# Optimization experiments

Hardware: AMD Instinct MI355X
Metric: run time of the kernel (lower is better)

Reference implementation:

```python
import jax, jax.numpy as jnp
import numpy as np
import math

B, T, D = 2, 2048, 1024
NH = 16
HD = D // NH


def setup_inputs() -> dict:
    key = jax.random.key(0)
    k1, k2, k3 = jax.random.split(key, 3)
    scale = 0.02
    x = jax.random.normal(k1, (B, T, D), dtype=jnp.float32)
    Wqkv = jax.random.normal(k2, (D, 3 * D), dtype=jnp.float32) * scale
    bqkv = jnp.zeros((3 * D,), dtype=jnp.float32)
    Wproj = jax.random.normal(k3, (D, D), dtype=jnp.float32) * scale
    bproj = jnp.zeros((D,), dtype=jnp.float32)
    return {"x": x, "Wqkv": Wqkv, "bqkv": bqkv, "Wproj": Wproj, "bproj": bproj}


def reference(x, Wqkv, bqkv, Wproj, bproj):
    b, t, c = x.shape
    qkv = x @ Wqkv + bqkv                      # [B,T,3D]
    q, k, v = jnp.split(qkv, 3, axis=2)
    # [B,T,NH,HD] -> [B,NH,T,HD]
    q = q.reshape(b, t, NH, HD).transpose(0, 2, 1, 3)
    k = k.reshape(b, t, NH, HD).transpose(0, 2, 1, 3)
    v = v.reshape(b, t, NH, HD).transpose(0, 2, 1, 3)
    att = jnp.einsum('bhqd,bhkd->bhqk', q, k) / math.sqrt(HD)  # [B,NH,T,T]
    causal = jnp.tril(jnp.ones((t, t), dtype=bool))
    att = jnp.where(causal, att, -jnp.inf)
    att = jax.nn.softmax(att, axis=-1)
    y = jnp.einsum('bhqk,bhkd->bhqd', att, v)  # [B,NH,T,HD]
    y = y.transpose(0, 2, 1, 3).reshape(b, t, c)
    return y @ Wproj + bproj
```

## Files before the change

kernel.cpp:

```cpp
#include <hip/hip_runtime.h>
#include <hip/hip_bf16.h>

#define B_   2
#define T_   2048
#define D_   1024
#define NH_  16
#define HD_  64
#define MROWS (B_*T_)
#define HEADELEMS (B_*NH_*T_*HD_)

#define QSCALE 0.180336880f

typedef unsigned short u16;
typedef unsigned int   u32;

typedef float f32x4  __attribute__((ext_vector_type(4)));
typedef short bf16x8 __attribute__((ext_vector_type(8)));

__device__ __forceinline__ float bf2f(u16 v) {
    return __uint_as_float(((u32)v) << 16);
}
__device__ __forceinline__ u16 f2bf(float f) {
    u32 x = __float_as_uint(f);
    u32 r = (x + 0x7fffu + ((x >> 16) & 1u)) >> 16;
    return (u16)r;
}

__global__ __launch_bounds__(256)
void conv_kernel(const float* __restrict__ in, u16* __restrict__ out, int n4)
{
    int i = blockIdx.x * 256 + threadIdx.x;
    if (i >= n4) return;
    float4 v = ((const float4*)in)[i];
    ushort4 o;
    o.x = f2bf(v.x); o.y = f2bf(v.y); o.z = f2bf(v.z); o.w = f2bf(v.w);
    ((ushort4*)out)[i] = o;
}

__global__ __launch_bounds__(256)
void transpose_conv_kernel(const float* __restrict__ in, u16* __restrict__ out,
                           int K, int N)
{
    __shared__ float Ts[64][65];
    const int t  = threadIdx.x;
    const int n0 = blockIdx.x * 64;
    const int k0 = blockIdx.y * 64;

    #pragma unroll
    for (int pass = 0; pass < 4; pass++) {
        const int r = pass * 16 + (t >> 4);
        const int c = (t & 15) * 4;
        float4 v = *(const float4*)(in + (size_t)(k0 + r) * N + n0 + c);
        Ts[r][c] = v.x; Ts[r][c+1] = v.y; Ts[r][c+2] = v.z; Ts[r][c+3] = v.w;
    }
    __syncthreads();
    #pragma unroll
    for (int pass = 0; pass < 2; pass++) {
        const int nn = pass * 32 + (t >> 3);
        const int kk = (t & 7) * 8;
        u16 o[8];
        #pragma unroll
        for (int j = 0; j < 8; j++) o[j] = f2bf(Ts[kk + j][nn]);
        *(uint4*)(out + (size_t)(n0 + nn) * K + k0 + kk) = *(const uint4*)o;
    }
}

template <int MODE>
__global__ __launch_bounds__(256)
void gemm_mfma(const u16* __restrict__ A, const u16* __restrict__ BT,
               const float* __restrict__ bias, void* __restrict__ outv,
               int M, int N, int K)
{
    __shared__ u16 As[128][40];
    __shared__ u16 Bs[128][40];

    const int t    = threadIdx.x;
    const int wave = t >> 6;
    const int lane = t & 63;
    const int l16  = lane & 15;
    const int quad = lane >> 4;

    const int m0 = blockIdx.y * 128;
    const int n0 = blockIdx.x * 128;
    const int mb = (wave >> 1) * 64;
    const int nb = (wave & 1) * 64;

    const int srow = t >> 2;
    const int skk  = (t & 3) * 8;

    f32x4 acc[4][4];
    #pragma unroll
    for (int i = 0; i < 4; i++)
        #pragma unroll
        for (int j = 0; j < 4; j++) acc[i][j] = (f32x4){0,0,0,0};

    for (int k0 = 0; k0 < K; k0 += 32) {
        __syncthreads();
        #pragma unroll
        for (int pass = 0; pass < 2; pass++) {
            const int r = srow + pass * 64;
            uint4 va = *(const uint4*)(A  + (size_t)(m0 + r) * K + k0 + skk);
            *(uint4*)&As[r][skk] = va;
            uint4 vb = *(const uint4*)(BT + (size_t)(n0 + r) * K + k0 + skk);
            *(uint4*)&Bs[r][skk] = vb;
        }
        __syncthreads();

        bf16x8 af[4], bfr[4];
        #pragma unroll
        for (int i = 0; i < 4; i++)
            af[i] = *(const bf16x8*)&As[mb + i*16 + l16][quad * 8];
        #pragma unroll
        for (int j = 0; j < 4; j++)
            bfr[j] = *(const bf16x8*)&Bs[nb + j*16 + l16][quad * 8];

        #pragma unroll
        for (int i = 0; i < 4; i++)
            #pragma unroll
            for (int j = 0; j < 4; j++)
                acc[i][j] = __builtin_amdgcn_mfma_f32_16x16x32_bf16(
                    af[i], bfr[j], acc[i][j], 0, 0, 0);
    }

    #pragma unroll
    for (int j = 0; j < 4; j++) {
        const int n = n0 + nb + j*16 + l16;
        const float bv = bias[n];
        #pragma unroll
        for (int i = 0; i < 4; i++) {
            #pragma unroll
            for (int r = 0; r < 4; r++) {
                const int m = m0 + mb + i*16 + quad*4 + r;
                float v = acc[i][j][r] + bv;
                if (MODE == 0) {
                    ((float*)outv)[(size_t)m * N + n] = v;
                } else {
                    const int b   = m >> 11;
                    const int tt  = m & 2047;
                    const int sec = n >> 10;
                    const int dd  = n & 1023;
                    const int h   = dd >> 6;
                    const int hd  = dd & 63;
                    const size_t hbase = ((size_t)(b*NH_ + h)) * T_ * HD_;
                    size_t idx;
                    if (sec == 2)
                        idx = (size_t)2 * HEADELEMS + hbase + (size_t)hd * T_ + tt;
                    else
                        idx = (size_t)sec * HEADELEMS + hbase + (size_t)tt * HD_ + hd;
                    if (sec == 0) v *= QSCALE;
                    ((u16*)outv)[idx] = f2bf(v);
                }
            }
        }
    }
}

__global__ __launch_bounds__(256)
void attn_mfma_kernel(const u16* __restrict__ Q, const u16* __restrict__ K,
                      const u16* __restrict__ VT, u16* __restrict__ y1)
{
    __shared__ u16 Ks[2][64][72];
    __shared__ u16 Vs[2][64][72];
    __shared__ u16 Plds[4][32][72];

    const int t    = threadIdx.x;
    const int wave = t >> 6;
    const int lane = t & 63;
    const int l16  = lane & 15;
    const int quad = lane >> 4;

    const int hb = blockIdx.x;
    const int yy = blockIdx.y;
    const int qt = (yy < 8) ? (15 - yy) : (yy - 8);
    const int b  = hb >> 4;
    const int h  = hb & 15;
    const size_t base = (size_t)hb * T_ * HD_;

    const int qw0 = qt * 128 + wave * 32;

    bf16x8 qf[2][2];
    #pragma unroll
    for (int mi = 0; mi < 2; mi++) {
        const u16* qp = Q + base + (size_t)(qw0 + mi*16 + l16) * HD_ + quad * 8;
        qf[mi][0] = *(const bf16x8*)(qp);
        qf[mi][1] = *(const bf16x8*)(qp + 32);
    }

    bf16x8 onesf;
    #pragma unroll
    for (int i = 0; i < 8; i++) onesf[i] = (short)0x3F80;

    f32x4 o[2][4];
    #pragma unroll
    for (int mi = 0; mi < 2; mi++)
        #pragma unroll
        for (int d = 0; d < 4; d++) o[mi][d] = (f32x4){0,0,0,0};
    f32x4 accl[2] = {(f32x4){0,0,0,0}, (f32x4){0,0,0,0}};

    u16 (*P)[72] = Plds[wave];

    const int nsteps  = 2 * qt + 2;
    const int tiles_w = (qw0 + 32 + 63) >> 6;

    const int srow = t >> 3;
    const int scol = (t & 7) * 8;

    uint4 kr0, kr1, vr0, vr1;
    {
        const u16* kp = K + base + (size_t)srow * HD_ + scol;
        kr0 = *(const uint4*)kp;
        kr1 = *(const uint4*)(kp + 32 * HD_);
        const u16* vp = VT + base + (size_t)srow * T_ + scol;
        vr0 = *(const uint4*)vp;
        vr1 = *(const uint4*)(vp + 32 * T_);
        *(uint4*)&Ks[0][srow][scol]      = kr0;
        *(uint4*)&Ks[0][srow + 32][scol] = kr1;
        *(uint4*)&Vs[0][srow][scol]      = vr0;
        *(uint4*)&Vs[0][srow + 32][scol] = vr1;
    }
    __syncthreads();

    for (int kt = 0; kt < nsteps; kt++) {
        const int cur = kt & 1;
        const int k0  = kt * 64;
        const bool have_next = (kt + 1 < nsteps);

        if (have_next) {
            const u16* kp = K + base + (size_t)(k0 + 64 + srow) * HD_ + scol;
            kr0 = *(const uint4*)kp;
            kr1 = *(const uint4*)(kp + 32 * HD_);
            const u16* vp = VT + base + (size_t)srow * T_ + k0 + 64 + scol;
            vr0 = *(const uint4*)vp;
            vr1 = *(const uint4*)(vp + 32 * T_);
        }

        if (kt < tiles_w) {
            f32x4 s[2][4];
            #pragma unroll
            for (int j = 0; j < 4; j++) {
                bf16x8 kf0 = *(const bf16x8*)&Ks[cur][j*16 + l16][quad * 8];
                bf16x8 kf1 = *(const bf16x8*)&Ks[cur][j*16 + l16][32 + quad * 8];
                #pragma unroll
                for (int mi = 0; mi < 2; mi++) {
                    f32x4 z = {0,0,0,0};
                    z = __builtin_amdgcn_mfma_f32_16x16x32_bf16(qf[mi][0], kf0, z, 0, 0, 0);
                    s[mi][j] = __builtin_amdgcn_mfma_f32_16x16x32_bf16(qf[mi][1], kf1, z, 0, 0, 0);
                }
            }

            #pragma unroll
            for (int mi = 0; mi < 2; mi++) {
                const int rmin = qw0 + mi * 16;
                const bool need_mask = (k0 + 63 > rmin);
                #pragma unroll
                for (int r = 0; r < 4; r++) {
                    const int qi = rmin + quad * 4 + r;
                    #pragma unroll
                    for (int j = 0; j < 4; j++) {
                        float e = __builtin_amdgcn_exp2f(s[mi][j][r]);
                        if (need_mask && (k0 + j*16 + l16 > qi)) e = 0.f;
                        P[mi*16 + quad*4 + r][j*16 + l16] =
                            (u16)((__float_as_uint(e) + 0x8000u) >> 16);
                    }
                }
            }

            bf16x8 pf[2][2];
            #pragma unroll
            for (int mi = 0; mi < 2; mi++) {
                pf[mi][0] = *(const bf16x8*)&P[mi*16 + l16][quad * 8];
                pf[mi][1] = *(const bf16x8*)&P[mi*16 + l16][32 + quad * 8];
            }

            #pragma unroll
            for (int mi = 0; mi < 2; mi++) {
                accl[mi] = __builtin_amdgcn_mfma_f32_16x16x32_bf16(pf[mi][0], onesf, accl[mi], 0, 0, 0);
                accl[mi] = __builtin_amdgcn_mfma_f32_16x16x32_bf16(pf[mi][1], onesf, accl[mi], 0, 0, 0);
            }

            #pragma unroll
            for (int d = 0; d < 4; d++) {
                bf16x8 v0 = *(const bf16x8*)&Vs[cur][d*16 + l16][quad * 8];
                bf16x8 v1 = *(const bf16x8*)&Vs[cur][d*16 + l16][32 + quad * 8];
                #pragma unroll
                for (int mi = 0; mi < 2; mi++) {
                    o[mi][d] = __builtin_amdgcn_mfma_f32_16x16x32_bf16(pf[mi][0], v0, o[mi][d], 0, 0, 0);
                    o[mi][d] = __builtin_amdgcn_mfma_f32_16x16x32_bf16(pf[mi][1], v1, o[mi][d], 0, 0, 0);
                }
            }
        }

        if (have_next) {
            const int nxt = cur ^ 1;
            *(uint4*)&Ks[nxt][srow][scol]      = kr0;
            *(uint4*)&Ks[nxt][srow + 32][scol] = kr1;
            *(uint4*)&Vs[nxt][srow][scol]      = vr0;
            *(uint4*)&Vs[nxt][srow + 32][scol] = vr1;
            __syncthreads();
        }
    }

    #pragma unroll
    for (int mi = 0; mi < 2; mi++) {
        #pragma unroll
        for (int r = 0; r < 4; r++) {
            const float inv = 1.f / accl[mi][r];
            const int qi = qw0 + mi*16 + quad*4 + r;
            u16* yp = y1 + ((size_t)(b * T_ + qi)) * D_ + h * HD_ + l16;
            yp[0]  = f2bf(o[mi][0][r] * inv);
            yp[16] = f2bf(o[mi][1][r] * inv);
            yp[32] = f2bf(o[mi][2][r] * inv);
            yp[48] = f2bf(o[mi][3][r] * inv);
        }
    }
}

extern "C" void kernel_launch(void* const* d_in, const int* in_sizes, int n_in,
                              void* d_out, int out_size, void* d_ws, size_t ws_size,
                              hipStream_t stream)
{
    const float* x     = (const float*)d_in[0];
    const float* Wqkv  = (const float*)d_in[1];
    const float* bqkv  = (const float*)d_in[2];
    const float* Wproj = (const float*)d_in[3];
    const float* bproj = (const float*)d_in[4];

    u16* scratch = (u16*)d_out;
    u16* xb      = scratch;
    u16* WqkvT   = scratch + (size_t)MROWS * D_;

    u16* qkv = (u16*)d_ws;
    u16* Qp  = qkv;
    u16* Kp  = qkv + (size_t)HEADELEMS;
    u16* Vtp = qkv + (size_t)2 * HEADELEMS;
    u16* y1b    = scratch;
    u16* WprojT = Kp;
    u16* y1c    = Vtp;

    conv_kernel<<<(MROWS*D_/4 + 255)/256, 256, 0, stream>>>(x, xb, MROWS*D_/4);

    transpose_conv_kernel<<<dim3(3*D_/64, D_/64), 256, 0, stream>>>(
        Wqkv, WqkvT, D_, 3*D_);

    gemm_mfma<1><<<dim3(3*D_/128, MROWS/128), 256, 0, stream>>>(
        xb, WqkvT, bqkv, (void*)qkv, MROWS, 3*D_, D_);

    attn_mfma_kernel<<<dim3(NH_*B_, T_/128), 256, 0, stream>>>(Qp, Kp, Vtp, y1b);

    transpose_conv_kernel<<<dim3(D_/64, D_/64), 256, 0, stream>>>(
        Wproj, WprojT, D_, D_);

    (void)hipMemcpyAsync(y1c, y1b, (size_t)MROWS * D_ * sizeof(u16),
                         hipMemcpyDeviceToDevice, stream);

    gemm_mfma<0><<<dim3(D_/128, MROWS/128), 256, 0, stream>>>(
        y1c, WprojT, bproj, d_out, MROWS, D_, D_);
}
```

Measured before the change: 228.2 us.

## Use direct global-to-LDS loads with swizzle in GEMM and transpose score MFMA

The GEMM tile loads now use global_load_lds to write straight into LDS, with an XOR swizzle replacing the padded layout to avoid bank conflicts. This removes the register staging round trip. In attention, the QK^T MFMA operands are swapped so each lane holds four consecutive key columns of one query row. That lets P be written as packed 64-bit stores instead of sixteen scalar 16-bit stores. The risk is that the LDS-direct load path and the swizzle mapping must match the fragment reads exactly.

```diff
diff --git a/kernel.cpp b/kernel.cpp
--- a/kernel.cpp
+++ b/kernel.cpp
@@ -17,6 +17,10 @@
 typedef float f32x4  __attribute__((ext_vector_type(4)));
 typedef short bf16x8 __attribute__((ext_vector_type(8)));
 
+#define GLP(g, l) __builtin_amdgcn_global_load_lds(                         \
+    (const __attribute__((address_space(1))) void*)(g),                     \
+    (__attribute__((address_space(3))) void*)(l), 16, 0, 0)
+
 __device__ __forceinline__ float bf2f(u16 v) {
     return __uint_as_float(((u32)v) << 16);
 }
@@ -71,8 +75,8 @@
                const float* __restrict__ bias, void* __restrict__ outv,
                int M, int N, int K)
 {
-    __shared__ u16 As[128][40];
-    __shared__ u16 Bs[128][40];
+    __shared__ u16 As[128][32];
+    __shared__ u16 Bs[128][32];
 
     const int t    = threadIdx.x;
     const int wave = t >> 6;
@@ -85,8 +89,19 @@
     const int mb = (wave >> 1) * 64;
     const int nb = (wave & 1) * 64;
 
-    const int srow = t >> 2;
-    const int skk  = (t & 3) * 8;
+    const int r0a  = wave * 16;
+    const int r0b  = 64 + wave * 16;
+    const int lr_a = r0a + (lane >> 2);
+    const int lr_b = r0b + (lane >> 2);
+    const int sega = (((lane & 3) ^ ((lr_a >> 1) & 3))) * 8;
+    const int segb = (((lane & 3) ^ ((lr_b >> 1) & 3))) * 8;
+
+    const u16* gA0 = A  + (size_t)(m0 + lr_a) * K + sega;
+    const u16* gA1 = A  + (size_t)(m0 + lr_b) * K + segb;
+    const u16* gB0 = BT + (size_t)(n0 + lr_a) * K + sega;
+    const u16* gB1 = BT + (size_t)(n0 + lr_b) * K + segb;
+
+    const int fragoff = (quad ^ ((l16 >> 1) & 3)) * 8;
 
     f32x4 acc[4][4];
     #pragma unroll
@@ -96,23 +111,19 @@
 
     for (int k0 = 0; k0 < K; k0 += 32) {
         __syncthreads();
-        #pragma unroll
-        for (int pass = 0; pass < 2; pass++) {
-            const int r = srow + pass * 64;
-            uint4 va = *(const uint4*)(A  + (size_t)(m0 + r) * K + k0 + skk);
-            *(uint4*)&As[r][skk] = va;
-            uint4 vb = *(const uint4*)(BT + (size_t)(n0 + r) * K + k0 + skk);
-            *(uint4*)&Bs[r][skk] = vb;
-        }
+        GLP(gA0 + k0, &As[r0a][0]);
+        GLP(gA1 + k0, &As[r0b][0]);
+        GLP(gB0 + k0, &Bs[r0a][0]);
+        GLP(gB1 + k0, &Bs[r0b][0]);
         __syncthreads();
 
         bf16x8 af[4], bfr[4];
         #pragma unroll
         for (int i = 0; i < 4; i++)
-            af[i] = *(const bf16x8*)&As[mb + i*16 + l16][quad * 8];
+            af[i] = *(const bf16x8*)&As[mb + i*16 + l16][fragoff];
         #pragma unroll
         for (int j = 0; j < 4; j++)
-            bfr[j] = *(const bf16x8*)&Bs[nb + j*16 + l16][quad * 8];
+            bfr[j] = *(const bf16x8*)&Bs[nb + j*16 + l16][fragoff];
 
         #pragma unroll
         for (int i = 0; i < 4; i++)
@@ -235,7 +246,7 @@
         }
 
         if (kt < tiles_w) {
-            f32x4 s[2][4];
+            f32x4 st[2][4];
             #pragma unroll
             for (int j = 0; j < 4; j++) {
                 bf16x8 kf0 = *(const bf16x8*)&Ks[cur][j*16 + l16][quad * 8];
@@ -243,25 +254,33 @@
                 #pragma unroll
                 for (int mi = 0; mi < 2; mi++) {
                     f32x4 z = {0,0,0,0};
-                    z = __builtin_amdgcn_mfma_f32_16x16x32_bf16(qf[mi][0], kf0, z, 0, 0, 0);
-                    s[mi][j] = __builtin_amdgcn_mfma_f32_16x16x32_bf16(qf[mi][1], kf1, z, 0, 0, 0);
+                    z = __builtin_amdgcn_mfma_f32_16x16x32_bf16(kf0, qf[mi][0], z, 0, 0, 0);
+                    st[mi][j] = __builtin_amdgcn_mfma_f32_16x16x32_bf16(kf1, qf[mi][1], z, 0, 0, 0);
                 }
             }
 
             #pragma unroll
             for (int mi = 0; mi < 2; mi++) {
-                const int rmin = qw0 + mi * 16;
-                const bool need_mask = (k0 + 63 > rmin);
+                const int qi = qw0 + mi*16 + l16;
+                const bool need_mask = (k0 + 63 > qw0 + mi*16);
                 #pragma unroll
-                for (int r = 0; r < 4; r++) {
-                    const int qi = rmin + quad * 4 + r;
-                    #pragma unroll
-                    for (int j = 0; j < 4; j++) {
-                        float e = __builtin_amdgcn_exp2f(s[mi][j][r]);
-                        if (need_mask && (k0 + j*16 + l16 > qi)) e = 0.f;
-                        P[mi*16 + quad*4 + r][j*16 + l16] =
-                            (u16)((__float_as_uint(e) + 0x8000u) >> 16);
+                for (int j = 0; j < 4; j++) {
+                    const int kb = k0 + j*16 + quad*4;
+                    float e0 = __builtin_amdgcn_exp2f(st[mi][j][0]);
+                    float e1 = __builtin_amdgcn_exp2f(st[mi][j][1]);
+                    float e2 = __builtin_amdgcn_exp2f(st[mi][j][2]);
+                    float e3 = __builtin_amdgcn_exp2f(st[mi][j][3]);
+                    if (need_mask) {
+                        if (kb + 0 > qi) e0 = 0.f;
+                        if (kb + 1 > qi) e1 = 0.f;
+                        if (kb + 2 > qi) e2 = 0.f;
+                        if (kb + 3 > qi) e3 = 0.f;
                     }
+                    u32 w0 = ((__float_as_uint(e0) + 0x8000u) >> 16)
+                           | ((__float_as_uint(e1) + 0x8000u) & 0xffff0000u);
+                    u32 w1 = ((__float_as_uint(e2) + 0x8000u) >> 16)
+                           | ((__float_as_uint(e3) + 0x8000u) & 0xffff0000u);
+                    *(uint2*)&P[mi*16 + l16][j*16 + quad*4] = make_uint2(w0, w1);
                 }
             }
 
```

Result: faster. 223.1 us (-2.3%).
